# Performance work log

Hardware: AMD Instinct MI355X
Metric: run time of the kernel (lower is better)

The kernel has to match this reference:

```python
import jax, jax.numpy as jnp
import numpy as np

B, N, G = 64, 100000, 256


def hat(w):
    # w: (...,3) -> skew-symmetric (...,3,3)
    z = jnp.zeros_like(w[..., 0])
    return jnp.stack([
        jnp.stack([z, -w[..., 2], w[..., 1]], -1),
        jnp.stack([w[..., 2], z, -w[..., 0]], -1),
        jnp.stack([-w[..., 1], w[..., 0], z], -1),
    ], -2)


def exp_se3(delta):
    # delta: (B,6) = [upsilon(3 trans), omega(3 rot)] -> (B,4,4) SE(3)
    ups, om = delta[:, :3], delta[:, 3:]
    th2 = jnp.sum(om * om, -1)
    th = jnp.sqrt(th2)
    small = th < 1e-6
    s = jnp.where(small, 1.0, th)  # safe theta
    A = jnp.where(small, 1.0 - th2 / 6.0, jnp.sin(s) / s)
    Bc = jnp.where(small, 0.5 - th2 / 24.0, (1.0 - jnp.cos(s)) / (s * s))
    Cc = jnp.where(small, 1.0 / 6.0 - th2 / 120.0, (s - jnp.sin(s)) / (s ** 3))
    K = hat(om)
    K2 = K @ K
    I = jnp.eye(3, dtype=delta.dtype)
    R = I + A[:, None, None] * K + Bc[:, None, None] * K2
    V = I + Bc[:, None, None] * K + Cc[:, None, None] * K2
    t = jnp.einsum('bij,bj->bi', V, ups)
    top = jnp.concatenate([R, t[:, :, None]], -1)            # (B,3,4)
    bot = jnp.broadcast_to(jnp.array([0., 0., 0., 1.], delta.dtype), (delta.shape[0], 1, 4))
    return jnp.concatenate([top, bot], 1)


def trilinear_sdf(grid, pts, limits):
    # grid: (Gx,Gy,Gz); pts: (B,N,3); limits: [xmin,ymin,zmin,xmax,ymax,zmax]
    Gx, Gy, Gz = grid.shape
    lo, hi = limits[:3], limits[3:]
    dims = jnp.array([Gx, Gy, Gz], pts.dtype)
    u = (pts - lo) / (hi - lo) * (dims - 1.0)
    u = jnp.clip(u, 0.0, dims - 1.0 - 1e-4)
    i0 = jnp.floor(u).astype(jnp.int32)
    f = u - i0.astype(pts.dtype)
    nmax = jnp.array([Gx - 1, Gy - 1, Gz - 1], jnp.int32)
    i1 = jnp.minimum(i0 + 1, nmax)
    flat = grid.reshape(-1)
    gather = lambda ix, iy, iz: flat[(ix * Gy + iy) * Gz + iz]
    x0, y0, z0 = i0[..., 0], i0[..., 1], i0[..., 2]
    x1, y1, z1 = i1[..., 0], i1[..., 1], i1[..., 2]
    fx, fy, fz = f[..., 0], f[..., 1], f[..., 2]
    c00 = gather(x0, y0, z0) * (1 - fx) + gather(x1, y0, z0) * fx
    c10 = gather(x0, y1, z0) * (1 - fx) + gather(x1, y1, z0) * fx
    c01 = gather(x0, y0, z1) * (1 - fx) + gather(x1, y0, z1) * fx
    c11 = gather(x0, y1, z1) * (1 - fx) + gather(x1, y1, z1) * fx
    c0 = c00 * (1 - fy) + c10 * fy
    c1 = c01 * (1 - fy) + c11 * fy
    return c0 * (1 - fz) + c1 * fz  # (B,N)


def setup_inputs() -> dict:
    key = jax.random.key(0)
    k1, k2, k3, k4 = jax.random.split(key, 4)
    pose_delta = 0.05 * jax.random.normal(k1, (B, 6), jnp.float32)
    # valid initial SE(3) poses built from random twists
    init_twist = 0.3 * jax.random.normal(k2, (B, 6), jnp.float32)
    pose_init = exp_se3(init_twist)
    sdf_grids = jax.random.normal(k3, (G, G, G), jnp.float32)
    sdf_limits = jnp.array([-0.5, -0.5, -0.5, 0.5, 0.5, 0.5], jnp.float32)
    points = jax.random.uniform(k4, (N, 3), jnp.float32, -0.4, 0.4)
    return {"pose_delta": pose_delta, "pose_init": pose_init,
            "sdf_grids": sdf_grids, "sdf_limits": sdf_limits, "points": points}


def reference(pose_delta, pose_init, sdf_grids, sdf_limits, points):
    se3 = exp_se3(pose_delta) @ pose_init                       # (B,4,4)
    p = jnp.einsum('bij,nj->bni', se3[:, :3, :3], points) + se3[:, None, :3, 3]  # (B,N,3)
    sdf_values = trilinear_sdf(sdf_grids, p, sdf_limits)        # (B,N)
    loss = 0.5 * jnp.sum(sdf_values ** 2)
    return loss, sdf_values, se3
```

## Files before the change

kernel.cpp:

```cpp
#include <hip/hip_runtime.h>
#include <hip/hip_fp16.h>
#include <math.h>


__global__ void pose_kernel(const float* __restrict__ pose_delta,
                            const float* __restrict__ pose_init,
                            float* __restrict__ out,
                            float* __restrict__ rt,
                            int B, long long se3_off)
{
    int b = blockIdx.x * blockDim.x + threadIdx.x;
    if (b == 0) out[0] = 0.0f;
    if (b >= B) return;

    const float* d = pose_delta + b * 6;
    float ux = d[0], uy = d[1], uz = d[2];
    float wx = d[3], wy = d[4], wz = d[5];
    float th2 = wx*wx + wy*wy + wz*wz;
    float th  = sqrtf(th2);
    float A, Bc, Cc;
    if (th < 1e-6f) {
        A  = 1.0f - th2 * (1.0f/6.0f);
        Bc = 0.5f - th2 * (1.0f/24.0f);
        Cc = (1.0f/6.0f) - th2 * (1.0f/120.0f);
    } else {
        float sn = sinf(th), cs = cosf(th);
        A  = sn / th;
        Bc = (1.0f - cs) / th2;
        Cc = (th - sn) / (th2 * th);
    }
    float K[3][3]  = {{0.f,-wz,wy},{wz,0.f,-wx},{-wy,wx,0.f}};
    float K2[3][3];
    #pragma unroll
    for (int i = 0; i < 3; i++)
        #pragma unroll
        for (int j = 0; j < 3; j++) {
            float s = 0.f;
            #pragma unroll
            for (int k = 0; k < 3; k++) s += K[i][k] * K[k][j];
            K2[i][j] = s;
        }
    float R[3][3], V[3][3];
    #pragma unroll
    for (int i = 0; i < 3; i++)
        #pragma unroll
        for (int j = 0; j < 3; j++) {
            float I = (i == j) ? 1.f : 0.f;
            R[i][j] = I + A  * K[i][j] + Bc * K2[i][j];
            V[i][j] = I + Bc * K[i][j] + Cc * K2[i][j];
        }
    float tt[3];
    #pragma unroll
    for (int i = 0; i < 3; i++)
        tt[i] = V[i][0]*ux + V[i][1]*uy + V[i][2]*uz;

    const float* P = pose_init + b * 16;
    float M[3][4];
    #pragma unroll
    for (int i = 0; i < 3; i++)
        #pragma unroll
        for (int j = 0; j < 4; j++)
            M[i][j] = R[i][0]*P[0*4+j] + R[i][1]*P[1*4+j] + R[i][2]*P[2*4+j] + tt[i]*P[3*4+j];

    float* o = out + se3_off + (long long)b * 16;
    #pragma unroll
    for (int i = 0; i < 3; i++)
        #pragma unroll
        for (int j = 0; j < 4; j++) o[i*4+j] = M[i][j];
    o[12] = P[12]; o[13] = P[13]; o[14] = P[14]; o[15] = P[15];

    float* r = rt + b * 12;
    #pragma unroll
    for (int i = 0; i < 3; i++) {
        r[i*4+0] = M[i][0]; r[i*4+1] = M[i][1];
        r[i*4+2] = M[i][2]; r[i*4+3] = M[i][3];
    }
}

__global__ __launch_bounds__(256)
void pack_zp(const float* __restrict__ g, uint2* __restrict__ tbl)
{
    int idx = blockIdx.x * 256 + threadIdx.x;
    int y = (idx >> 8) & 255;
    int ys = (y < 255) ? 256 : 0;
    const float* p = g + idx;
    float e00 = p[0],          e10 = p[65536];
    float e01 = p[ys],         e11 = p[65536 + ys];
    uint2 u;
    __half2 h;
    h = __floats2half2_rn(e00, e10); u.x = *(unsigned int*)&h;
    h = __floats2half2_rn(e01, e11); u.y = *(unsigned int*)&h;
    tbl[idx] = u;
}

__global__ __launch_bounds__(256)
void sdf_zp4(const uint2* __restrict__ tbl,
             const float* __restrict__ limits,
             const float* __restrict__ points,
             const float* __restrict__ rt,
             float* __restrict__ sdf_out,
             float* __restrict__ partials,
             int N, int B)
{
    const int bg = blockIdx.y;
    const int b0 = bg * 4;
    const int n  = blockIdx.x * 256 + threadIdx.x;

    float M[4][12];
    #pragma unroll
    for (int bb = 0; bb < 4; bb++) {
        int b = min(b0 + bb, B - 1);
        const float* m = rt + b * 12;
        #pragma unroll
        for (int j = 0; j < 12; j++) M[bb][j] = m[j];
    }
    float lo0=limits[0], lo1=limits[1], lo2=limits[2];
    float hi0=limits[3], hi1=limits[4], hi2=limits[5];
    float s0 = 255.0f/(hi0-lo0), s1 = 255.0f/(hi1-lo1), s2 = 255.0f/(hi2-lo2);

    float val = 0.0f;
    if (n < N) {
        float px = points[n*3+0], py = points[n*3+1], pz = points[n*3+2];

        int   idx[4];
        float fx[4], fy[4], fz[4];
        #pragma unroll
        for (int bb = 0; bb < 4; bb++) {
            float x = M[bb][0]*px + M[bb][1]*py + M[bb][2]*pz  + M[bb][3];
            float y = M[bb][4]*px + M[bb][5]*py + M[bb][6]*pz  + M[bb][7];
            float z = M[bb][8]*px + M[bb][9]*py + M[bb][10]*pz + M[bb][11];
            float u0 = fminf(fmaxf((x - lo0) * s0, 0.f), 254.9999f);
            float u1 = fminf(fmaxf((y - lo1) * s1, 0.f), 254.9999f);
            float u2 = fminf(fmaxf((z - lo2) * s2, 0.f), 254.9999f);
            int x0 = (int)u0, y0 = (int)u1, z0 = (int)u2;
            fx[bb] = u0 - (float)x0;
            fy[bb] = u1 - (float)y0;
            fz[bb] = u2 - (float)z0;
            idx[bb] = (x0 << 16) | (y0 << 8) | z0;
        }

        uint2 e0[4], e1[4];
        #pragma unroll
        for (int bb = 0; bb < 4; bb++) {
            e0[bb] = tbl[idx[bb]];
            e1[bb] = tbl[idx[bb] + 1];
        }

        #pragma unroll
        for (int bb = 0; bb < 4; bb++) {
            float2 a00 = __half22float2(*(__half2*)&e0[bb].x);
            float2 a01 = __half22float2(*(__half2*)&e0[bb].y);
            float2 b00 = __half22float2(*(__half2*)&e1[bb].x);
            float2 b01 = __half22float2(*(__half2*)&e1[bb].y);
            float c0 = a00.x + (a00.y - a00.x) * fx[bb];
            float c1 = a01.x + (a01.y - a01.x) * fx[bb];
            float p0 = c0 + (c1 - c0) * fy[bb];
            float d0 = b00.x + (b00.y - b00.x) * fx[bb];
            float d1 = b01.x + (b01.y - b01.x) * fx[bb];
            float p1 = d0 + (d1 - d0) * fy[bb];
            float v  = p0 + (p1 - p0) * fz[bb];
            if (b0 + bb < B) {
                sdf_out[(size_t)(b0 + bb) * N + n] = v;
                val += v * v;
            }
        }
    }

    #pragma unroll
    for (int off = 32; off > 0; off >>= 1) val += __shfl_down(val, off, 64);
    __shared__ float sm[4];
    int lane = threadIdx.x & 63, wid = threadIdx.x >> 6;
    if (lane == 0) sm[wid] = val;
    __syncthreads();
    if (threadIdx.x == 0)
        partials[(size_t)bg * gridDim.x + blockIdx.x] = sm[0] + sm[1] + sm[2] + sm[3];
}

__global__ __launch_bounds__(1024)
void reduce_kernel(const float* __restrict__ partials, int n, float* __restrict__ out)
{
    float s = 0.f;
    for (int i = threadIdx.x; i < n; i += 1024) s += partials[i];
    #pragma unroll
    for (int off = 32; off > 0; off >>= 1) s += __shfl_down(s, off, 64);
    __shared__ float sm[16];
    int lane = threadIdx.x & 63, wid = threadIdx.x >> 6;
    if (lane == 0) sm[wid] = s;
    __syncthreads();
    if (threadIdx.x == 0) {
        float t = 0.f;
        #pragma unroll
        for (int i = 0; i < 16; i++) t += sm[i];
        out[0] = 0.5f * t;
    }
}

__global__ __launch_bounds__(256)
void sdf_kernel(const float* __restrict__ grid,
                const float* __restrict__ limits,
                const float* __restrict__ points,
                const float* __restrict__ rt,
                float* __restrict__ out, int N)
{
    const int b = blockIdx.y;
    const int n = blockIdx.x * 256 + threadIdx.x;
    const float* m = rt + b * 12;
    float m00=m[0], m01=m[1], m02=m[2],  m03=m[3];
    float m10=m[4], m11=m[5], m12=m[6],  m13=m[7];
    float m20=m[8], m21=m[9], m22=m[10], m23=m[11];
    float lo0=limits[0], lo1=limits[1], lo2=limits[2];
    float hi0=limits[3], hi1=limits[4], hi2=limits[5];
    float s0 = 255.0f/(hi0-lo0), s1 = 255.0f/(hi1-lo1), s2 = 255.0f/(hi2-lo2);

    float val = 0.0f;
    if (n < N) {
        float px = points[n*3+0], py = points[n*3+1], pz = points[n*3+2];
        float x = m00*px + m01*py + m02*pz + m03;
        float y = m10*px + m11*py + m12*pz + m13;
        float z = m20*px + m21*py + m22*pz + m23;
        float u0 = fminf(fmaxf((x - lo0) * s0, 0.f), 254.9999f);
        float u1 = fminf(fmaxf((y - lo1) * s1, 0.f), 254.9999f);
        float u2 = fminf(fmaxf((z - lo2) * s2, 0.f), 254.9999f);
        int x0 = (int)u0, y0 = (int)u1, z0 = (int)u2;
        float fx = u0 - (float)x0, fy = u1 - (float)y0, fz = u2 - (float)z0;
        int x1 = x0 + 1, y1 = y0 + 1, z1 = z0 + 1;
        int bx0 = x0 << 16, bx1 = x1 << 16;
        int by0 = y0 << 8,  by1 = y1 << 8;
        float g000 = grid[bx0|by0|z0], g100 = grid[bx1|by0|z0];
        float g010 = grid[bx0|by1|z0], g110 = grid[bx1|by1|z0];
        float g001 = grid[bx0|by0|z1], g101 = grid[bx1|by0|z1];
        float g011 = grid[bx0|by1|z1], g111 = grid[bx1|by1|z1];
        float c00 = g000*(1.f-fx) + g100*fx;
        float c10 = g010*(1.f-fx) + g110*fx;
        float c01 = g001*(1.f-fx) + g101*fx;
        float c11 = g011*(1.f-fx) + g111*fx;
        float c0  = c00*(1.f-fy) + c10*fy;
        float c1  = c01*(1.f-fy) + c11*fy;
        float v   = c0*(1.f-fz) + c1*fz;
        out[1 + (size_t)b * N + n] = v;
        val = v * v;
    }
    #pragma unroll
    for (int off = 32; off > 0; off >>= 1) val += __shfl_down(val, off, 64);
    __shared__ float sm[4];
    int lane = threadIdx.x & 63, wid = threadIdx.x >> 6;
    if (lane == 0) sm[wid] = val;
    __syncthreads();
    if (threadIdx.x == 0)
        atomicAdd(out, 0.5f * (sm[0] + sm[1] + sm[2] + sm[3]));
}

extern "C" void kernel_launch(void* const* d_in, const int* in_sizes, int n_in,
                              void* d_out, int out_size, void* d_ws, size_t ws_size,
                              hipStream_t stream) {
    const float* pose_delta = (const float*)d_in[0];
    const float* pose_init  = (const float*)d_in[1];
    const float* grid       = (const float*)d_in[2];
    const float* limits     = (const float*)d_in[3];
    const float* points     = (const float*)d_in[4];
    float* out = (float*)d_out;

    int B = in_sizes[0] / 6;
    int N = in_sizes[4] / 3;
    long long se3_off = 1 + (long long)B * N;

    const size_t TBL_OFF = 131072;
    const size_t needZP = TBL_OFF + (size_t)255 * 65536 * 8;
    float* rt       = (float*)d_ws;
    float* partials = (float*)((char*)d_ws + 4096);
    void*  tbl      = (void*)((char*)d_ws + TBL_OFF);

    pose_kernel<<<1, ((B + 63) / 64) * 64, 0, stream>>>(pose_delta, pose_init, out, rt, B, se3_off);

    bool g256 = (in_sizes[2] == (1 << 24));
    int gridX = (N + 255) / 256;

    if (g256 && ws_size >= needZP) {
        int nBG = (B + 3) / 4;
        pack_zp<<<255 * 65536 / 256, 256, 0, stream>>>(grid, (uint2*)tbl);
        dim3 g(gridX, nBG);
        sdf_zp4<<<g, 256, 0, stream>>>((const uint2*)tbl, limits, points, rt,
                                       out + 1, partials, N, B);
        reduce_kernel<<<1, 1024, 0, stream>>>(partials, nBG * gridX, out);
    } else {
        dim3 g(gridX, B);
        sdf_kernel<<<g, 256, 0, stream>>>(grid, limits, points, rt, out, N);
    }
}
```

Before: 150.1 us.

## Fuse pose computation into pack kernel and replace reduce kernel with atomics

Folds the per-batch pose computation into the first block of the grid-packing kernel and drops the separate reduction kernel. Each SDF block now atomically adds its scaled partial sum into the loss. SDF outputs are written with nontemporal stores. Together these cut two kernel launches and avoid polluting cache with streaming output, at the cost of nondeterministic float summation order and heavy atomic traffic on a single address.

```diff
diff --git a/kernel.cpp b/kernel.cpp
--- a/kernel.cpp
+++ b/kernel.cpp
@@ -3,16 +3,12 @@
 #include <math.h>
 
 
-__global__ void pose_kernel(const float* __restrict__ pose_delta,
-                            const float* __restrict__ pose_init,
-                            float* __restrict__ out,
-                            float* __restrict__ rt,
-                            int B, long long se3_off)
-{
-    int b = blockIdx.x * blockDim.x + threadIdx.x;
-    if (b == 0) out[0] = 0.0f;
-    if (b >= B) return;
-
+__device__ __forceinline__ void pose_math(const float* __restrict__ pose_delta,
+                                          const float* __restrict__ pose_init,
+                                          float* __restrict__ out,
+                                          float* __restrict__ rt,
+                                          int b, long long se3_off)
+{
     const float* d = pose_delta + b * 6;
     float ux = d[0], uy = d[1], uz = d[2];
     float wx = d[3], wy = d[4], wz = d[5];
@@ -78,7 +74,11 @@
 }
 
 __global__ __launch_bounds__(256)
-void pack_zp(const float* __restrict__ g, uint2* __restrict__ tbl)
+void pack_pose(const float* __restrict__ g, uint2* __restrict__ tbl,
+               const float* __restrict__ pose_delta,
+               const float* __restrict__ pose_init,
+               float* __restrict__ out, float* __restrict__ rt,
+               int B, long long se3_off)
 {
     int idx = blockIdx.x * 256 + threadIdx.x;
     int y = (idx >> 8) & 255;
@@ -91,6 +91,12 @@
     h = __floats2half2_rn(e00, e10); u.x = *(unsigned int*)&h;
     h = __floats2half2_rn(e01, e11); u.y = *(unsigned int*)&h;
     tbl[idx] = u;
+
+    if (blockIdx.x == 0) {
+        if (threadIdx.x == 0) out[0] = 0.0f;
+        if ((int)threadIdx.x < B)
+            pose_math(pose_delta, pose_init, out, rt, threadIdx.x, se3_off);
+    }
 }
 
 __global__ __launch_bounds__(256)
@@ -99,7 +105,7 @@
              const float* __restrict__ points,
              const float* __restrict__ rt,
              float* __restrict__ sdf_out,
-             float* __restrict__ partials,
+             float* __restrict__ loss,
              int N, int B)
 {
     const int bg = blockIdx.y;
@@ -160,7 +166,7 @@
             float p1 = d0 + (d1 - d0) * fy[bb];
             float v  = p0 + (p1 - p0) * fz[bb];
             if (b0 + bb < B) {
-                sdf_out[(size_t)(b0 + bb) * N + n] = v;
+                __builtin_nontemporal_store(v, &sdf_out[(size_t)(b0 + bb) * N + n]);
                 val += v * v;
             }
         }
@@ -173,26 +179,19 @@
     if (lane == 0) sm[wid] = val;
     __syncthreads();
     if (threadIdx.x == 0)
-        partials[(size_t)bg * gridDim.x + blockIdx.x] = sm[0] + sm[1] + sm[2] + sm[3];
-}
-
-__global__ __launch_bounds__(1024)
-void reduce_kernel(const float* __restrict__ partials, int n, float* __restrict__ out)
-{
-    float s = 0.f;
-    for (int i = threadIdx.x; i < n; i += 1024) s += partials[i];
-    #pragma unroll
-    for (int off = 32; off > 0; off >>= 1) s += __shfl_down(s, off, 64);
-    __shared__ float sm[16];
-    int lane = threadIdx.x & 63, wid = threadIdx.x >> 6;
-    if (lane == 0) sm[wid] = s;
-    __syncthreads();
-    if (threadIdx.x == 0) {
-        float t = 0.f;
-        #pragma unroll
-        for (int i = 0; i < 16; i++) t += sm[i];
-        out[0] = 0.5f * t;
-    }
+        atomicAdd(loss, 0.5f * (sm[0] + sm[1] + sm[2] + sm[3]));
+}
+
+__global__ void pose_kernel(const float* __restrict__ pose_delta,
+                            const float* __restrict__ pose_init,
+                            float* __restrict__ out,
+                            float* __restrict__ rt,
+                            int B, long long se3_off)
+{
+    int b = blockIdx.x * blockDim.x + threadIdx.x;
+    if (b == 0) out[0] = 0.0f;
+    if (b >= B) return;
+    pose_math(pose_delta, pose_init, out, rt, b, se3_off);
 }
 
 __global__ __launch_bounds__(256)
@@ -266,23 +265,21 @@
 
     const size_t TBL_OFF = 131072;
     const size_t needZP = TBL_OFF + (size_t)255 * 65536 * 8;
-    float* rt       = (float*)d_ws;
-    float* partials = (float*)((char*)d_ws + 4096);
-    void*  tbl      = (void*)((char*)d_ws + TBL_OFF);
-
-    pose_kernel<<<1, ((B + 63) / 64) * 64, 0, stream>>>(pose_delta, pose_init, out, rt, B, se3_off);
+    float* rt  = (float*)d_ws;
+    uint2* tbl = (uint2*)((char*)d_ws + TBL_OFF);
 
     bool g256 = (in_sizes[2] == (1 << 24));
     int gridX = (N + 255) / 256;
 
-    if (g256 && ws_size >= needZP) {
+    if (g256 && ws_size >= needZP && B <= 256) {
+        pack_pose<<<255 * 65536 / 256, 256, 0, stream>>>(grid, tbl, pose_delta,
+                                                         pose_init, out, rt, B, se3_off);
         int nBG = (B + 3) / 4;
-        pack_zp<<<255 * 65536 / 256, 256, 0, stream>>>(grid, (uint2*)tbl);
         dim3 g(gridX, nBG);
-        sdf_zp4<<<g, 256, 0, stream>>>((const uint2*)tbl, limits, points, rt,
-                                       out + 1, partials, N, B);
-        reduce_kernel<<<1, 1024, 0, stream>>>(partials, nBG * gridX, out);
+        sdf_zp4<<<g, 256, 0, stream>>>(tbl, limits, points, rt, out + 1, out, N, B);
     } else {
+        pose_kernel<<<1, ((B + 63) / 64) * 64, 0, stream>>>(pose_delta, pose_init,
+                                                            out, rt, B, se3_off);
         dim3 g(gridX, B);
         sdf_kernel<<<g, 256, 0, stream>>>(grid, limits, points, rt, out, N);
     }
```

After: 159.7 us. 1.06x slower.
